# Optimization experiments

Measured on AMD Instinct MI355X. Metric: run time of the kernel, lower is better.

## Reference

```python
import jax, jax.numpy as jnp
import numpy as np

EMBED_DIM = 1024
NUM_HEADS = 16
HEAD_DIM = EMBED_DIM // NUM_HEADS
B, S = 4, 2048
LN_EPS = 1e-6


def setup_inputs() -> dict:
    key = jax.random.key(0)
    ks = jax.random.split(key, 11)
    sc = 1.0 / np.sqrt(EMBED_DIM)
    inputs = jax.random.normal(ks[0], (B, S, EMBED_DIM), dtype=jnp.float32)
    Wq = jax.random.normal(ks[1], (EMBED_DIM, EMBED_DIM), dtype=jnp.float32) * sc
    bq = jnp.zeros((EMBED_DIM,), jnp.float32)
    Wk = jax.random.normal(ks[2], (EMBED_DIM, EMBED_DIM), dtype=jnp.float32) * sc
    bk = jnp.zeros((EMBED_DIM,), jnp.float32)
    Wv = jax.random.normal(ks[3], (EMBED_DIM, EMBED_DIM), dtype=jnp.float32) * sc
    bv = jnp.zeros((EMBED_DIM,), jnp.float32)
    Wo = jax.random.normal(ks[4], (EMBED_DIM, EMBED_DIM), dtype=jnp.float32) * sc
    bo = jnp.zeros((EMBED_DIM,), jnp.float32)
    gamma = jnp.ones((EMBED_DIM,), jnp.float32)
    beta = jnp.zeros((EMBED_DIM,), jnp.float32)
    return {"inputs": inputs, "Wq": Wq, "bq": bq, "Wk": Wk, "bk": bk,
            "Wv": Wv, "bv": bv, "Wo": Wo, "bo": bo, "gamma": gamma, "beta": beta}


def _attention(inputs, Wq, bq, Wk, bk, Wv, bv, Wo, bo, gamma, beta):
    b, s, d = inputs.shape
    q = (inputs @ Wq + bq).reshape(b, s, NUM_HEADS, HEAD_DIM)
    k = (inputs @ Wk + bk).reshape(b, s, NUM_HEADS, HEAD_DIM)
    v = (inputs @ Wv + bv).reshape(b, s, NUM_HEADS, HEAD_DIM)
    scale = jnp.float32(np.sqrt(HEAD_DIM))
    # [b, h, s, s]
    scores = jnp.einsum('bqhd,bkhd->bhqk', q, k) / scale
    causal = jnp.tril(jnp.ones((s, s), dtype=bool))  # [s, s]
    scores = jnp.where(causal, scores, jnp.float32(-1e9))
    weights = jax.nn.softmax(scores, axis=-1)
    # dropout is identity at inference (training=False)
    attn = jnp.einsum('bhqk,bkhd->bqhd', weights, v).reshape(b, s, d)
    out = attn @ Wo + bo
    resid = inputs + out
    mu = jnp.mean(resid, axis=-1, keepdims=True)
    var = jnp.mean(jnp.square(resid - mu), axis=-1, keepdims=True)
    normed = (resid - mu) / jnp.sqrt(var + LN_EPS) * gamma + beta
    return normed, weights


def reference(inputs, Wq, bq, Wk, bk, Wv, bv, Wo, bo, gamma, beta):
    return _attention(inputs, Wq, bq, Wk, bk, Wv, bv, Wo, bo, gamma, beta)
```

## Files before the change

kernel.cpp:

```cpp
#include <hip/hip_runtime.h>
#include <math.h>

#define B_  4
#define S_  2048
#define D_  1024
#define H_  16
#define DH_ 64
#define M_  (B_*S_)
#define LN_EPS 1e-6f

typedef __attribute__((ext_vector_type(4))) float f32x4;
typedef __attribute__((ext_vector_type(8))) short s16x8;

__device__ __forceinline__ void split2(float x, ushort& h, ushort& l) {
  unsigned u = __float_as_uint(x);
  h = (ushort)(u >> 16);
  float r = x - __uint_as_float(u & 0xFFFF0000u);
  l = (ushort)(__float_as_uint(r) >> 16);
}

__global__ __launch_bounds__(256) void split_kernel(
    const float* __restrict__ in, ushort* __restrict__ hi, ushort* __restrict__ lo)
{
  const size_t t = (size_t)blockIdx.x * 256 + threadIdx.x;
  const float4 a = *(const float4*)(in + t * 8);
  const float4 b = *(const float4*)(in + t * 8 + 4);
  s16x8 hv, lv;
  ushort h, l;
  split2(a.x, h, l); hv[0] = (short)h; lv[0] = (short)l;
  split2(a.y, h, l); hv[1] = (short)h; lv[1] = (short)l;
  split2(a.z, h, l); hv[2] = (short)h; lv[2] = (short)l;
  split2(a.w, h, l); hv[3] = (short)h; lv[3] = (short)l;
  split2(b.x, h, l); hv[4] = (short)h; lv[4] = (short)l;
  split2(b.y, h, l); hv[5] = (short)h; lv[5] = (short)l;
  split2(b.z, h, l); hv[6] = (short)h; lv[6] = (short)l;
  split2(b.w, h, l); hv[7] = (short)h; lv[7] = (short)l;
  *(s16x8*)(hi + t * 8) = hv;
  *(s16x8*)(lo + t * 8) = lv;
}

__global__ __launch_bounds__(256) void splitT_kernel(
    const float* __restrict__ W, ushort* __restrict__ hiT, ushort* __restrict__ loT)
{
  __shared__ float tile[64][65];
  const int n0 = blockIdx.x * 64, k0 = blockIdx.y * 64;
  const int tid = threadIdx.x;
  #pragma unroll
  for (int i = 0; i < 4; ++i) {
    int c = tid + (i << 8);
    int r = c >> 4;
    int c4 = (c & 15) << 2;
    float4 v = *(const float4*)(W + (size_t)(k0 + r) * D_ + n0 + c4);
    tile[r][c4+0] = v.x; tile[r][c4+1] = v.y; tile[r][c4+2] = v.z; tile[r][c4+3] = v.w;
  }
  __syncthreads();
  #pragma unroll
  for (int i = 0; i < 4; ++i) {
    int c = tid + (i << 8);
    int n = c >> 4;
    int k4 = (c & 15) << 2;
    ushort h0,h1,h2,h3, l0,l1,l2,l3;
    split2(tile[k4+0][n], h0, l0);
    split2(tile[k4+1][n], h1, l1);
    split2(tile[k4+2][n], h2, l2);
    split2(tile[k4+3][n], h3, l3);
    size_t o = (size_t)(n0 + n) * D_ + k0 + k4;
    *(ushort4*)(hiT + o) = make_ushort4(h0, h1, h2, h3);
    *(ushort4*)(loT + o) = make_ushort4(l0, l1, l2, l3);
  }
}

#define LDK 40

__global__ __launch_bounds__(256) void gemm_mfma_kernel(
    const ushort* __restrict__ Ahi, const ushort* __restrict__ Alo,
    const ushort* __restrict__ BThi, const ushort* __restrict__ BTlo,
    const float* __restrict__ bias, const float* __restrict__ resid,
    float* __restrict__ C, int M, int N, int K)
{
  __shared__ ushort Ah[128][LDK];
  __shared__ ushort Al[128][LDK];
  __shared__ ushort Bh[128][LDK];
  __shared__ ushort Bl[128][LDK];
  const int tid  = threadIdx.x;
  const int lane = tid & 63;
  const int wid  = tid >> 6;
  const int wm   = wid >> 1, wn = wid & 1;
  const int bm = blockIdx.y * 128, bn = blockIdx.x * 128;

  const int c0 = tid,       r0 = c0 >> 2, k80 = (c0 & 3) << 3;
  const int c1 = tid + 256, r1 = c1 >> 2, k81 = (c1 & 3) << 3;

  f32x4 acc[4][4] = {};

  const int kf = (lane >> 4) << 3;
  const int fm = wm * 64 + (lane & 15);
  const int fn = wn * 64 + (lane & 15);

  for (int k0 = 0; k0 < K; k0 += 32) {
    const size_t ga0 = (size_t)(bm + r0) * K + k0 + k80;
    const size_t ga1 = (size_t)(bm + r1) * K + k0 + k81;
    const size_t gb0 = (size_t)(bn + r0) * K + k0 + k80;
    const size_t gb1 = (size_t)(bn + r1) * K + k0 + k81;
    s16x8 va0 = *(const s16x8*)(Ahi  + ga0);
    s16x8 va1 = *(const s16x8*)(Ahi  + ga1);
    s16x8 ua0 = *(const s16x8*)(Alo  + ga0);
    s16x8 ua1 = *(const s16x8*)(Alo  + ga1);
    s16x8 vb0 = *(const s16x8*)(BThi + gb0);
    s16x8 vb1 = *(const s16x8*)(BThi + gb1);
    s16x8 ub0 = *(const s16x8*)(BTlo + gb0);
    s16x8 ub1 = *(const s16x8*)(BTlo + gb1);
    *(s16x8*)&Ah[r0][k80] = va0;  *(s16x8*)&Ah[r1][k81] = va1;
    *(s16x8*)&Al[r0][k80] = ua0;  *(s16x8*)&Al[r1][k81] = ua1;
    *(s16x8*)&Bh[r0][k80] = vb0;  *(s16x8*)&Bh[r1][k81] = vb1;
    *(s16x8*)&Bl[r0][k80] = ub0;  *(s16x8*)&Bl[r1][k81] = ub1;
    __syncthreads();
    s16x8 ah[4], al[4], bh[4], bl[4];
    #pragma unroll
    for (int i = 0; i < 4; ++i) {
      ah[i] = *(const s16x8*)&Ah[fm + i*16][kf];
      al[i] = *(const s16x8*)&Al[fm + i*16][kf];
      bh[i] = *(const s16x8*)&Bh[fn + i*16][kf];
      bl[i] = *(const s16x8*)&Bl[fn + i*16][kf];
    }
    #pragma unroll
    for (int mi = 0; mi < 4; ++mi) {
      #pragma unroll
      for (int ni = 0; ni < 4; ++ni) {
        acc[mi][ni] = __builtin_amdgcn_mfma_f32_16x16x32_bf16(ah[mi], bh[ni], acc[mi][ni], 0, 0, 0);
        acc[mi][ni] = __builtin_amdgcn_mfma_f32_16x16x32_bf16(al[mi], bh[ni], acc[mi][ni], 0, 0, 0);
        acc[mi][ni] = __builtin_amdgcn_mfma_f32_16x16x32_bf16(ah[mi], bl[ni], acc[mi][ni], 0, 0, 0);
      }
    }
    __syncthreads();
  }
  const int rbase = bm + wm*64 + ((lane >> 4) << 2);
  #pragma unroll
  for (int ni = 0; ni < 4; ++ni) {
    const int col = bn + wn*64 + ni*16 + (lane & 15);
    const float bb = bias[col];
    #pragma unroll
    for (int mi = 0; mi < 4; ++mi) {
      #pragma unroll
      for (int j = 0; j < 4; ++j) {
        const int row = rbase + mi*16 + j;
        float v = acc[mi][ni][j] + bb;
        if (resid) v += resid[(size_t)row * N + col];
        C[(size_t)row * N + col] = v;
      }
    }
  }
}

__device__ __forceinline__ float block_allreduce(float v, bool is_max, float* sbuf) {
  #pragma unroll
  for (int o = 32; o > 0; o >>= 1) {
    float other = __shfl_down(v, o, 64);
    v = is_max ? fmaxf(v, other) : (v + other);
  }
  __syncthreads();
  if ((threadIdx.x & 63) == 0) sbuf[threadIdx.x >> 6] = v;
  __syncthreads();
  float r = sbuf[0];
  #pragma unroll
  for (int w = 1; w < 4; ++w) r = is_max ? fmaxf(r, sbuf[w]) : (r + sbuf[w]);
  return r;
}

__global__ __launch_bounds__(256) void scores_kernel(
    const float* __restrict__ Q, const float* __restrict__ Km,
    float* __restrict__ Wout)
{
  const int kt = blockIdx.x, qt = blockIdx.y;
  if (kt > qt) return;
  const int bh = blockIdx.z;
  const int b = bh >> 4, h = bh & 15;
  const int q0 = qt * 64, k0 = kt * 64;
  __shared__ float Qs[64][68];
  __shared__ float Ks[64][68];
  const int tid = threadIdx.x;
  const int tx = tid & 15, ty = tid >> 4;
  const float* Qbase = Q  + ((size_t)b * S_ + q0) * D_ + h * DH_;
  const float* Kbase = Km + ((size_t)b * S_ + k0) * D_ + h * DH_;
  #pragma unroll
  for (int i = 0; i < 4; ++i) {
    int idx = tid + i * 256;
    int r = idx >> 4;
    int c4 = (idx & 15) << 2;
    float4 qv = *(const float4*)(Qbase + (size_t)r * D_ + c4);
    *(float4*)(&Qs[r][c4]) = qv;
    float4 kv = *(const float4*)(Kbase + (size_t)r * D_ + c4);
    Ks[c4+0][r] = kv.x; Ks[c4+1][r] = kv.y; Ks[c4+2][r] = kv.z; Ks[c4+3][r] = kv.w;
  }
  __syncthreads();
  float acc[4][4] = {};
  #pragma unroll 8
  for (int d = 0; d < 64; ++d) {
    float4 kv = *(float4*)(&Ks[d][tx*4]);
    float a0 = Qs[ty*4+0][d], a1 = Qs[ty*4+1][d];
    float a2 = Qs[ty*4+2][d], a3 = Qs[ty*4+3][d];
    acc[0][0] += a0*kv.x; acc[0][1] += a0*kv.y; acc[0][2] += a0*kv.z; acc[0][3] += a0*kv.w;
    acc[1][0] += a1*kv.x; acc[1][1] += a1*kv.y; acc[1][2] += a1*kv.z; acc[1][3] += a1*kv.w;
    acc[2][0] += a2*kv.x; acc[2][1] += a2*kv.y; acc[2][2] += a2*kv.z; acc[2][3] += a2*kv.w;
    acc[3][0] += a3*kv.x; acc[3][1] += a3*kv.y; acc[3][2] += a3*kv.z; acc[3][3] += a3*kv.w;
  }
  const float scale = 0.125f;
  float* Wrow = Wout + ((size_t)bh * S_ + q0) * S_ + k0;
  if (kt < qt) {
    #pragma unroll
    for (int i = 0; i < 4; ++i) {
      float4 o;
      o.x = acc[i][0]*scale; o.y = acc[i][1]*scale;
      o.z = acc[i][2]*scale; o.w = acc[i][3]*scale;
      *(float4*)(Wrow + (size_t)(ty*4+i) * S_ + tx*4) = o;
    }
  } else {
    #pragma unroll
    for (int i = 0; i < 4; ++i) {
      int qg = q0 + ty*4 + i;
      #pragma unroll
      for (int j = 0; j < 4; ++j) {
        int kg = k0 + tx*4 + j;
        if (kg <= qg) Wrow[(size_t)(ty*4+i) * S_ + tx*4 + j] = acc[i][j] * scale;
      }
    }
  }
}

__global__ __launch_bounds__(256) void softmax_kernel(float* __restrict__ Wbuf) {
  const int q = blockIdx.x;
  float* row = Wbuf + ((size_t)blockIdx.y * S_ + q) * S_;
  const int valid = q + 1;
  __shared__ float sbuf[4];
  float v[8];
  float lmax = -INFINITY;
  #pragma unroll
  for (int i = 0; i < 8; ++i) {
    int k = threadIdx.x + (i << 8);
    v[i] = (k < valid) ? row[k] : -INFINITY;
    lmax = fmaxf(lmax, v[i]);
  }
  float m = block_allreduce(lmax, true, sbuf);
  float lsum = 0.f;
  #pragma unroll
  for (int i = 0; i < 8; ++i) {
    int k = threadIdx.x + (i << 8);
    v[i] = (k < valid) ? __expf(v[i] - m) : 0.f;
    lsum += v[i];
  }
  float s = block_allreduce(lsum, false, sbuf);
  float inv = 1.f / s;
  #pragma unroll
  for (int i = 0; i < 8; ++i) {
    int k = threadIdx.x + (i << 8);
    row[k] = v[i] * inv;
  }
}

__global__ __launch_bounds__(256) void pv_kernel(
    const float* __restrict__ Wbuf, const float* __restrict__ V,
    float* __restrict__ Attn)
{
  const int qt = blockIdx.x, h = blockIdx.y, b = blockIdx.z;
  const int q0 = qt * 64;
  __shared__ float Ws[64][68];
  __shared__ float Vs[64][68];
  const int tid = threadIdx.x;
  const int tx = tid & 15, ty = tid >> 4;
  float acc[4][4] = {};
  const size_t wbase = (((size_t)b * H_ + h) * S_ + q0) * S_;
  const float* Vbase = V + (size_t)b * S_ * D_ + h * DH_;
  for (int kt = 0; kt <= qt; ++kt) {
    int k0 = kt * 64;
    #pragma unroll
    for (int i = 0; i < 4; ++i) {
      int idx = tid + i * 256;
      int r = idx >> 4, c4 = (idx & 15) << 2;
      *(float4*)(&Ws[r][c4]) = *(const float4*)(Wbuf + wbase + (size_t)r * S_ + k0 + c4);
      *(float4*)(&Vs[r][c4]) = *(const float4*)(Vbase + (size_t)(k0 + r) * D_ + c4);
    }
    __syncthreads();
    #pragma unroll 8
    for (int kk = 0; kk < 64; ++kk) {
      float4 vv = *(float4*)(&Vs[kk][tx*4]);
      float w0 = Ws[ty*4+0][kk], w1 = Ws[ty*4+1][kk];
      float w2 = Ws[ty*4+2][kk], w3 = Ws[ty*4+3][kk];
      acc[0][0] += w0*vv.x; acc[0][1] += w0*vv.y; acc[0][2] += w0*vv.z; acc[0][3] += w0*vv.w;
      acc[1][0] += w1*vv.x; acc[1][1] += w1*vv.y; acc[1][2] += w1*vv.z; acc[1][3] += w1*vv.w;
      acc[2][0] += w2*vv.x; acc[2][1] += w2*vv.y; acc[2][2] += w2*vv.z; acc[2][3] += w2*vv.w;
      acc[3][0] += w3*vv.x; acc[3][1] += w3*vv.y; acc[3][2] += w3*vv.z; acc[3][3] += w3*vv.w;
    }
    __syncthreads();
  }
  #pragma unroll
  for (int i = 0; i < 4; ++i) {
    float4 o = { acc[i][0], acc[i][1], acc[i][2], acc[i][3] };
    *(float4*)(Attn + ((size_t)b * S_ + q0 + ty*4 + i) * D_ + h * DH_ + tx*4) = o;
  }
}

__global__ __launch_bounds__(256) void ln_kernel(
    const float* __restrict__ R, const float* __restrict__ gamma,
    const float* __restrict__ beta, float* __restrict__ Out)
{
  const int row = blockIdx.x;
  const float* x = R + (size_t)row * D_;
  __shared__ float sbuf[4];
  float4 xv = *(const float4*)(x + threadIdx.x * 4);
  float s  = xv.x + xv.y + xv.z + xv.w;
  float ss = xv.x*xv.x + xv.y*xv.y + xv.z*xv.z + xv.w*xv.w;
  float tot  = block_allreduce(s,  false, sbuf);
  float tot2 = block_allreduce(ss, false, sbuf);
  float mu  = tot  * (1.f / D_);
  float var = tot2 * (1.f / D_) - mu * mu;
  float inv = rsqrtf(var + LN_EPS);
  float4 g  = *(const float4*)(gamma + threadIdx.x * 4);
  float4 be = *(const float4*)(beta  + threadIdx.x * 4);
  float4 o;
  o.x = (xv.x - mu) * inv * g.x + be.x;
  o.y = (xv.y - mu) * inv * g.y + be.y;
  o.z = (xv.z - mu) * inv * g.z + be.z;
  o.w = (xv.w - mu) * inv * g.w + be.w;
  *(float4*)(Out + (size_t)row * D_ + threadIdx.x * 4) = o;
}

extern "C" void kernel_launch(void* const* d_in, const int* in_sizes, int n_in,
                              void* d_out, int out_size, void* d_ws, size_t ws_size,
                              hipStream_t stream) {
  const float* X     = (const float*)d_in[0];
  const float* Wq    = (const float*)d_in[1];
  const float* bq    = (const float*)d_in[2];
  const float* Wk    = (const float*)d_in[3];
  const float* bk    = (const float*)d_in[4];
  const float* Wv    = (const float*)d_in[5];
  const float* bv    = (const float*)d_in[6];
  const float* Wo    = (const float*)d_in[7];
  const float* bo    = (const float*)d_in[8];
  const float* gamma = (const float*)d_in[9];
  const float* beta  = (const float*)d_in[10];

  float* out     = (float*)d_out;
  float* normed  = out;
  float* weights = out + (size_t)B_ * S_ * D_;

  const size_t sz = (size_t)B_ * S_ * D_;
  const size_t wsz = (size_t)D_ * D_;
  float* ws   = (float*)d_ws;
  float* Qb   = ws;
  float* Kb   = ws + sz;
  float* Vb   = ws + 2 * sz;
  float* Attn  = Qb;
  float* Resid = Kb;

  ushort* Xhi  = (ushort*)weights;
  ushort* Xlo  = Xhi + sz;
  ushort* WqHi = Xlo + sz;      ushort* WqLo = WqHi + wsz;
  ushort* WkHi = WqLo + wsz;    ushort* WkLo = WkHi + wsz;
  ushort* WvHi = WkLo + wsz;    ushort* WvLo = WvHi + wsz;
  ushort* AtHi = (ushort*)Vb;   ushort* AtLo = AtHi + sz;
  ushort* WoHi = (ushort*)Qb;   ushort* WoLo = WoHi + wsz;

  dim3 blk(256);
  dim3 gg(D_ / 128, M_ / 128);
  dim3 sg(sz / 2048);

  split_kernel <<<sg, blk, 0, stream>>>(X, Xhi, Xlo);
  splitT_kernel<<<dim3(16,16), blk, 0, stream>>>(Wq, WqHi, WqLo);
  splitT_kernel<<<dim3(16,16), blk, 0, stream>>>(Wk, WkHi, WkLo);
  splitT_kernel<<<dim3(16,16), blk, 0, stream>>>(Wv, WvHi, WvLo);

  gemm_mfma_kernel<<<gg, blk, 0, stream>>>(Xhi, Xlo, WqHi, WqLo, bq, nullptr, Qb, M_, D_, D_);
  gemm_mfma_kernel<<<gg, blk, 0, stream>>>(Xhi, Xlo, WkHi, WkLo, bk, nullptr, Kb, M_, D_, D_);
  gemm_mfma_kernel<<<gg, blk, 0, stream>>>(Xhi, Xlo, WvHi, WvLo, bv, nullptr, Vb, M_, D_, D_);

  scores_kernel<<<dim3(S_/64, S_/64, B_*H_), blk, 0, stream>>>(Qb, Kb, weights);
  softmax_kernel<<<dim3(S_, B_*H_), blk, 0, stream>>>(weights);
  pv_kernel<<<dim3(S_/64, H_, B_), blk, 0, stream>>>(weights, Vb, Attn);

  split_kernel <<<sg, blk, 0, stream>>>(Attn, AtHi, AtLo);
  splitT_kernel<<<dim3(16,16), blk, 0, stream>>>(Wo, WoHi, WoLo);
  gemm_mfma_kernel<<<gg, blk, 0, stream>>>(AtHi, AtLo, WoHi, WoLo, bo, X, Resid, M_, D_, D_);

  ln_kernel<<<dim3(M_), blk, 0, stream>>>(Resid, gamma, beta, normed);
}
```

Measured before the change: 2.339 ms.

## Move attention scores and PV products to split-bf16 MFMA kernels

Replaces the scalar FP32 scores and PV kernels with MFMA versions. Each fp32 operand is split into bf16 hi and lo parts in shared memory and combined with three MFMAs to keep near-fp32 accuracy. Query tiles grow to 128 rows, with the causal mask handled per 64-wide key tile. This trades FMA-bound compute for matrix-core throughput, at the cost of extra split arithmetic, more LDS traffic and scattered scalar stores for the output.

```diff
diff --git a/kernel.cpp b/kernel.cpp
--- a/kernel.cpp
+++ b/kernel.cpp
@@ -167,61 +167,100 @@
   return r;
 }
 
-__global__ __launch_bounds__(256) void scores_kernel(
+#define SQP 72
+
+__global__ __launch_bounds__(256) void scores_mfma_kernel(
     const float* __restrict__ Q, const float* __restrict__ Km,
     float* __restrict__ Wout)
 {
-  const int kt = blockIdx.x, qt = blockIdx.y;
-  if (kt > qt) return;
+  const int kt = blockIdx.x;
+  const int qt = blockIdx.y;
+  if (kt > 2*qt + 1) return;
   const int bh = blockIdx.z;
   const int b = bh >> 4, h = bh & 15;
-  const int q0 = qt * 64, k0 = kt * 64;
-  __shared__ float Qs[64][68];
-  __shared__ float Ks[64][68];
+  const int q0 = qt * 128, k0 = kt * 64;
+  __shared__ ushort Qh[128][SQP], Ql[128][SQP];
+  __shared__ ushort Kh[64][SQP],  Kl[64][SQP];
   const int tid = threadIdx.x;
-  const int tx = tid & 15, ty = tid >> 4;
+  const int lane = tid & 63, wid = tid >> 6;
+  const int wm = wid >> 1, wn = wid & 1;
   const float* Qbase = Q  + ((size_t)b * S_ + q0) * D_ + h * DH_;
   const float* Kbase = Km + ((size_t)b * S_ + k0) * D_ + h * DH_;
   #pragma unroll
+  for (int i = 0; i < 8; ++i) {
+    int idx = tid + (i << 8);
+    int r = idx >> 4, c4 = (idx & 15) << 2;
+    float4 v = *(const float4*)(Qbase + (size_t)r * D_ + c4);
+    ushort h0,h1,h2,h3,l0,l1,l2,l3;
+    split2(v.x,h0,l0); split2(v.y,h1,l1); split2(v.z,h2,l2); split2(v.w,h3,l3);
+    *(ushort4*)&Qh[r][c4] = make_ushort4(h0,h1,h2,h3);
+    *(ushort4*)&Ql[r][c4] = make_ushort4(l0,l1,l2,l3);
+  }
+  #pragma unroll
   for (int i = 0; i < 4; ++i) {
-    int idx = tid + i * 256;
-    int r = idx >> 4;
-    int c4 = (idx & 15) << 2;
-    float4 qv = *(const float4*)(Qbase + (size_t)r * D_ + c4);
-    *(float4*)(&Qs[r][c4]) = qv;
-    float4 kv = *(const float4*)(Kbase + (size_t)r * D_ + c4);
-    Ks[c4+0][r] = kv.x; Ks[c4+1][r] = kv.y; Ks[c4+2][r] = kv.z; Ks[c4+3][r] = kv.w;
+    int idx = tid + (i << 8);
+    int r = idx >> 4, c4 = (idx & 15) << 2;
+    float4 v = *(const float4*)(Kbase + (size_t)r * D_ + c4);
+    ushort h0,h1,h2,h3,l0,l1,l2,l3;
+    split2(v.x,h0,l0); split2(v.y,h1,l1); split2(v.z,h2,l2); split2(v.w,h3,l3);
+    *(ushort4*)&Kh[r][c4] = make_ushort4(h0,h1,h2,h3);
+    *(ushort4*)&Kl[r][c4] = make_ushort4(l0,l1,l2,l3);
   }
   __syncthreads();
-  float acc[4][4] = {};
-  #pragma unroll 8
-  for (int d = 0; d < 64; ++d) {
-    float4 kv = *(float4*)(&Ks[d][tx*4]);
-    float a0 = Qs[ty*4+0][d], a1 = Qs[ty*4+1][d];
-    float a2 = Qs[ty*4+2][d], a3 = Qs[ty*4+3][d];
-    acc[0][0] += a0*kv.x; acc[0][1] += a0*kv.y; acc[0][2] += a0*kv.z; acc[0][3] += a0*kv.w;
-    acc[1][0] += a1*kv.x; acc[1][1] += a1*kv.y; acc[1][2] += a1*kv.z; acc[1][3] += a1*kv.w;
-    acc[2][0] += a2*kv.x; acc[2][1] += a2*kv.y; acc[2][2] += a2*kv.z; acc[2][3] += a2*kv.w;
-    acc[3][0] += a3*kv.x; acc[3][1] += a3*kv.y; acc[3][2] += a3*kv.z; acc[3][3] += a3*kv.w;
+  const int kf = (lane >> 4) << 3;
+  const int fm = wm * 64 + (lane & 15);
+  const int fn = wn * 32 + (lane & 15);
+  f32x4 acc[4][2] = {};
+  #pragma unroll
+  for (int d0 = 0; d0 < 64; d0 += 32) {
+    s16x8 qa[4], qb[4], ka[2], kb[2];
+    #pragma unroll
+    for (int mi = 0; mi < 4; ++mi) {
+      qa[mi] = *(const s16x8*)&Qh[fm + mi*16][d0 + kf];
+      qb[mi] = *(const s16x8*)&Ql[fm + mi*16][d0 + kf];
+    }
+    #pragma unroll
+    for (int ni = 0; ni < 2; ++ni) {
+      ka[ni] = *(const s16x8*)&Kh[fn + ni*16][d0 + kf];
+      kb[ni] = *(const s16x8*)&Kl[fn + ni*16][d0 + kf];
+    }
+    #pragma unroll
+    for (int mi = 0; mi < 4; ++mi) {
+      #pragma unroll
+      for (int ni = 0; ni < 2; ++ni) {
+        acc[mi][ni] = __builtin_amdgcn_mfma_f32_16x16x32_bf16(qa[mi], ka[ni], acc[mi][ni], 0, 0, 0);
+        acc[mi][ni] = __builtin_amdgcn_mfma_f32_16x16x32_bf16(qb[mi], ka[ni], acc[mi][ni], 0, 0, 0);
+        acc[mi][ni] = __builtin_amdgcn_mfma_f32_16x16x32_bf16(qa[mi], kb[ni], acc[mi][ni], 0, 0, 0);
+      }
+    }
   }
   const float scale = 0.125f;
   float* Wrow = Wout + ((size_t)bh * S_ + q0) * S_ + k0;
-  if (kt < qt) {
-    #pragma unroll
-    for (int i = 0; i < 4; ++i) {
-      float4 o;
-      o.x = acc[i][0]*scale; o.y = acc[i][1]*scale;
-      o.z = acc[i][2]*scale; o.w = acc[i][3]*scale;
-      *(float4*)(Wrow + (size_t)(ty*4+i) * S_ + tx*4) = o;
+  const int rb = wm*64 + ((lane >> 4) << 2);
+  if ((kt >> 1) < qt) {
+    #pragma unroll
+    for (int ni = 0; ni < 2; ++ni) {
+      const int col = wn*32 + ni*16 + (lane & 15);
+      #pragma unroll
+      for (int mi = 0; mi < 4; ++mi) {
+        #pragma unroll
+        for (int j = 0; j < 4; ++j)
+          Wrow[(size_t)(rb + mi*16 + j) * S_ + col] = acc[mi][ni][j] * scale;
+      }
     }
   } else {
     #pragma unroll
-    for (int i = 0; i < 4; ++i) {
-      int qg = q0 + ty*4 + i;
-      #pragma unroll
-      for (int j = 0; j < 4; ++j) {
-        int kg = k0 + tx*4 + j;
-        if (kg <= qg) Wrow[(size_t)(ty*4+i) * S_ + tx*4 + j] = acc[i][j] * scale;
+    for (int ni = 0; ni < 2; ++ni) {
+      const int col = wn*32 + ni*16 + (lane & 15);
+      const int kg = k0 + col;
+      #pragma unroll
+      for (int mi = 0; mi < 4; ++mi) {
+        #pragma unroll
+        for (int j = 0; j < 4; ++j) {
+          const int row = rb + mi*16 + j;
+          if (kg <= q0 + row)
+            Wrow[(size_t)row * S_ + col] = acc[mi][ni][j] * scale;
+        }
       }
     }
   }
@@ -257,45 +296,85 @@
   }
 }
 
-__global__ __launch_bounds__(256) void pv_kernel(
+#define PVW 72
+#define PVV 74
+
+__global__ __launch_bounds__(256) void pv_mfma_kernel(
     const float* __restrict__ Wbuf, const float* __restrict__ V,
     float* __restrict__ Attn)
 {
   const int qt = blockIdx.x, h = blockIdx.y, b = blockIdx.z;
-  const int q0 = qt * 64;
-  __shared__ float Ws[64][68];
-  __shared__ float Vs[64][68];
+  const int q0 = qt * 128;
+  __shared__ ushort Wh[128][PVW], Wl[128][PVW];
+  __shared__ ushort Vh[64][PVV],  Vl[64][PVV];
   const int tid = threadIdx.x;
-  const int tx = tid & 15, ty = tid >> 4;
-  float acc[4][4] = {};
+  const int lane = tid & 63, wid = tid >> 6;
+  const int wm = wid >> 1, wn = wid & 1;
+  f32x4 acc[4][2] = {};
   const size_t wbase = (((size_t)b * H_ + h) * S_ + q0) * S_;
   const float* Vbase = V + (size_t)b * S_ * D_ + h * DH_;
-  for (int kt = 0; kt <= qt; ++kt) {
-    int k0 = kt * 64;
+  const int kf = (lane >> 4) << 3;
+  const int fm = wm * 64 + (lane & 15);
+  const int fn = wn * 32 + (lane & 15);
+  const int nkt = 2*qt + 2;
+  for (int kt = 0; kt < nkt; ++kt) {
+    const int k0 = kt * 64;
+    #pragma unroll
+    for (int i = 0; i < 8; ++i) {
+      int idx = tid + (i << 8);
+      int r = idx >> 4, c4 = (idx & 15) << 2;
+      float4 v = *(const float4*)(Wbuf + wbase + (size_t)r * S_ + k0 + c4);
+      ushort h0,h1,h2,h3,l0,l1,l2,l3;
+      split2(v.x,h0,l0); split2(v.y,h1,l1); split2(v.z,h2,l2); split2(v.w,h3,l3);
+      *(ushort4*)&Wh[r][c4] = make_ushort4(h0,h1,h2,h3);
+      *(ushort4*)&Wl[r][c4] = make_ushort4(l0,l1,l2,l3);
+    }
     #pragma unroll
     for (int i = 0; i < 4; ++i) {
-      int idx = tid + i * 256;
+      int idx = tid + (i << 8);
       int r = idx >> 4, c4 = (idx & 15) << 2;
-      *(float4*)(&Ws[r][c4]) = *(const float4*)(Wbuf + wbase + (size_t)r * S_ + k0 + c4);
-      *(float4*)(&Vs[r][c4]) = *(const float4*)(Vbase + (size_t)(k0 + r) * D_ + c4);
+      float4 v = *(const float4*)(Vbase + (size_t)(k0 + r) * D_ + c4);
+      ushort h0,h1,h2,h3,l0,l1,l2,l3;
+      split2(v.x,h0,l0); split2(v.y,h1,l1); split2(v.z,h2,l2); split2(v.w,h3,l3);
+      Vh[c4+0][r] = h0; Vh[c4+1][r] = h1; Vh[c4+2][r] = h2; Vh[c4+3][r] = h3;
+      Vl[c4+0][r] = l0; Vl[c4+1][r] = l1; Vl[c4+2][r] = l2; Vl[c4+3][r] = l3;
     }
     __syncthreads();
-    #pragma unroll 8
-    for (int kk = 0; kk < 64; ++kk) {
-      float4 vv = *(float4*)(&Vs[kk][tx*4]);
-      float w0 = Ws[ty*4+0][kk], w1 = Ws[ty*4+1][kk];
-      float w2 = Ws[ty*4+2][kk], w3 = Ws[ty*4+3][kk];
-      acc[0][0] += w0*vv.x; acc[0][1] += w0*vv.y; acc[0][2] += w0*vv.z; acc[0][3] += w0*vv.w;
-      acc[1][0] += w1*vv.x; acc[1][1] += w1*vv.y; acc[1][2] += w1*vv.z; acc[1][3] += w1*vv.w;
-      acc[2][0] += w2*vv.x; acc[2][1] += w2*vv.y; acc[2][2] += w2*vv.z; acc[2][3] += w2*vv.w;
-      acc[3][0] += w3*vv.x; acc[3][1] += w3*vv.y; acc[3][2] += w3*vv.z; acc[3][3] += w3*vv.w;
+    #pragma unroll
+    for (int kk = 0; kk < 64; kk += 32) {
+      s16x8 wa[4], wb[4], va[2], vb[2];
+      #pragma unroll
+      for (int mi = 0; mi < 4; ++mi) {
+        wa[mi] = *(const s16x8*)&Wh[fm + mi*16][kk + kf];
+        wb[mi] = *(const s16x8*)&Wl[fm + mi*16][kk + kf];
+      }
+      #pragma unroll
+      for (int ni = 0; ni < 2; ++ni) {
+        va[ni] = *(const s16x8*)&Vh[fn + ni*16][kk + kf];
+        vb[ni] = *(const s16x8*)&Vl[fn + ni*16][kk + kf];
+      }
+      #pragma unroll
+      for (int mi = 0; mi < 4; ++mi) {
+        #pragma unroll
+        for (int ni = 0; ni < 2; ++ni) {
+          acc[mi][ni] = __builtin_amdgcn_mfma_f32_16x16x32_bf16(wa[mi], va[ni], acc[mi][ni], 0, 0, 0);
+          acc[mi][ni] = __builtin_amdgcn_mfma_f32_16x16x32_bf16(wb[mi], va[ni], acc[mi][ni], 0, 0, 0);
+          acc[mi][ni] = __builtin_amdgcn_mfma_f32_16x16x32_bf16(wa[mi], vb[ni], acc[mi][ni], 0, 0, 0);
+        }
+      }
     }
     __syncthreads();
   }
-  #pragma unroll
-  for (int i = 0; i < 4; ++i) {
-    float4 o = { acc[i][0], acc[i][1], acc[i][2], acc[i][3] };
-    *(float4*)(Attn + ((size_t)b * S_ + q0 + ty*4 + i) * D_ + h * DH_ + tx*4) = o;
+  const int rb = q0 + wm*64 + ((lane >> 4) << 2);
+  #pragma unroll
+  for (int ni = 0; ni < 2; ++ni) {
+    const int col = h * DH_ + wn*32 + ni*16 + (lane & 15);
+    #pragma unroll
+    for (int mi = 0; mi < 4; ++mi) {
+      #pragma unroll
+      for (int j = 0; j < 4; ++j)
+        Attn[((size_t)b * S_ + rb + mi*16 + j) * D_ + col] = acc[mi][ni][j];
+    }
   }
 }
 
@@ -373,9 +452,9 @@
   gemm_mfma_kernel<<<gg, blk, 0, stream>>>(Xhi, Xlo, WkHi, WkLo, bk, nullptr, Kb, M_, D_, D_);
   gemm_mfma_kernel<<<gg, blk, 0, stream>>>(Xhi, Xlo, WvHi, WvLo, bv, nullptr, Vb, M_, D_, D_);
 
-  scores_kernel<<<dim3(S_/64, S_/64, B_*H_), blk, 0, stream>>>(Qb, Kb, weights);
+  scores_mfma_kernel<<<dim3(S_/64, S_/128, B_*H_), blk, 0, stream>>>(Qb, Kb, weights);
   softmax_kernel<<<dim3(S_, B_*H_), blk, 0, stream>>>(weights);
-  pv_kernel<<<dim3(S_/64, H_, B_), blk, 0, stream>>>(weights, Vb, Attn);
+  pv_mfma_kernel<<<dim3(S_/128, H_, B_), blk, 0, stream>>>(weights, Vb, Attn);
 
   split_kernel <<<sg, blk, 0, stream>>>(Attn, AtHi, AtLo);
   splitT_kernel<<<dim3(16,16), blk, 0, stream>>>(Wo, WoHi, WoLo);
```

Measured after the change: 2.122 ms. 1.1x faster.

## Fuse scores, softmax and PV into flash-style MFMA attention kernel; async LDS loads in GEMM

Applied to the files above, without the earlier changes.

Replaces the separate scores, softmax and PV kernels with one flash-attention style kernel. It uses split-bf16 MFMA for QK^T and PV with an online softmax, then recomputes the scores in a second pass to write the normalized weights and zero the masked region. This avoids writing, rereading and rewriting the full score matrix across three kernels, at the cost of computing QK^T twice. The GEMM also switches to global_load_lds direct-to-LDS loads without padding, which may add LDS bank conflicts. Note that Attn aliases Qb, but each block reads only its own Q rows into registers before writing Attn.

```diff
diff --git a/kernel.cpp b/kernel.cpp
--- a/kernel.cpp
+++ b/kernel.cpp
@@ -11,6 +11,12 @@
 
 typedef __attribute__((ext_vector_type(4))) float f32x4;
 typedef __attribute__((ext_vector_type(8))) short s16x8;
+
+__device__ __forceinline__ void gl16(const void* g, void* l) {
+  __builtin_amdgcn_global_load_lds(
+      (const __attribute__((address_space(1))) unsigned int*)g,
+      (__attribute__((address_space(3))) unsigned int*)l, 16, 0, 0);
+}
 
 __device__ __forceinline__ void split2(float x, ushort& h, ushort& l) {
   unsigned u = __float_as_uint(x);
@@ -70,50 +76,48 @@
   }
 }
 
-#define LDK 40
-
 __global__ __launch_bounds__(256) void gemm_mfma_kernel(
     const ushort* __restrict__ Ahi, const ushort* __restrict__ Alo,
     const ushort* __restrict__ BThi, const ushort* __restrict__ BTlo,
     const float* __restrict__ bias, const float* __restrict__ resid,
     float* __restrict__ C, int M, int N, int K)
 {
-  __shared__ ushort Ah[128][LDK];
-  __shared__ ushort Al[128][LDK];
-  __shared__ ushort Bh[128][LDK];
-  __shared__ ushort Bl[128][LDK];
+  __shared__ ushort Ah[128][32], Al[128][32], Bh[128][32], Bl[128][32];
   const int tid  = threadIdx.x;
   const int lane = tid & 63;
   const int wid  = tid >> 6;
   const int wm   = wid >> 1, wn = wid & 1;
   const int bm = blockIdx.y * 128, bn = blockIdx.x * 128;
 
-  const int c0 = tid,       r0 = c0 >> 2, k80 = (c0 & 3) << 3;
-  const int c1 = tid + 256, r1 = c1 >> 2, k81 = (c1 & 3) << 3;
+  const int j0 = wid * 128 + lane, j1 = j0 + 64;
+  const int r0 = j0 >> 2, kc0 = (j0 & 3) << 3;
+  const int r1 = j1 >> 2, kc1 = (j1 & 3) << 3;
+  const unsigned off0 = (unsigned)(wid * 128) * 16;
+  const unsigned off1 = off0 + 1024;
+
+  const ushort* a0  = Ahi  + (size_t)(bm + r0) * K + kc0;
+  const ushort* a1  = Ahi  + (size_t)(bm + r1) * K + kc1;
+  const ushort* c0  = Alo  + (size_t)(bm + r0) * K + kc0;
+  const ushort* c1  = Alo  + (size_t)(bm + r1) * K + kc1;
+  const ushort* b0  = BThi + (size_t)(bn + r0) * K + kc0;
+  const ushort* b1  = BThi + (size_t)(bn + r1) * K + kc1;
+  const ushort* d0p = BTlo + (size_t)(bn + r0) * K + kc0;
+  const ushort* d1p = BTlo + (size_t)(bn + r1) * K + kc1;
 
   f32x4 acc[4][4] = {};
-
   const int kf = (lane >> 4) << 3;
   const int fm = wm * 64 + (lane & 15);
   const int fn = wn * 64 + (lane & 15);
 
   for (int k0 = 0; k0 < K; k0 += 32) {
-    const size_t ga0 = (size_t)(bm + r0) * K + k0 + k80;
-    const size_t ga1 = (size_t)(bm + r1) * K + k0 + k81;
-    const size_t gb0 = (size_t)(bn + r0) * K + k0 + k80;
-    const size_t gb1 = (size_t)(bn + r1) * K + k0 + k81;
-    s16x8 va0 = *(const s16x8*)(Ahi  + ga0);
-    s16x8 va1 = *(const s16x8*)(Ahi  + ga1);
-    s16x8 ua0 = *(const s16x8*)(Alo  + ga0);
-    s16x8 ua1 = *(const s16x8*)(Alo  + ga1);
-    s16x8 vb0 = *(const s16x8*)(BThi + gb0);
-    s16x8 vb1 = *(const s16x8*)(BThi + gb1);
-    s16x8 ub0 = *(const s16x8*)(BTlo + gb0);
-    s16x8 ub1 = *(const s16x8*)(BTlo + gb1);
-    *(s16x8*)&Ah[r0][k80] = va0;  *(s16x8*)&Ah[r1][k81] = va1;
-    *(s16x8*)&Al[r0][k80] = ua0;  *(s16x8*)&Al[r1][k81] = ua1;
-    *(s16x8*)&Bh[r0][k80] = vb0;  *(s16x8*)&Bh[r1][k81] = vb1;
-    *(s16x8*)&Bl[r0][k80] = ub0;  *(s16x8*)&Bl[r1][k81] = ub1;
+    gl16(a0 + k0,  (char*)&Ah[0][0] + off0);
+    gl16(a1 + k0,  (char*)&Ah[0][0] + off1);
+    gl16(c0 + k0,  (char*)&Al[0][0] + off0);
+    gl16(c1 + k0,  (char*)&Al[0][0] + off1);
+    gl16(b0 + k0,  (char*)&Bh[0][0] + off0);
+    gl16(b1 + k0,  (char*)&Bh[0][0] + off1);
+    gl16(d0p + k0, (char*)&Bl[0][0] + off0);
+    gl16(d1p + k0, (char*)&Bl[0][0] + off1);
     __syncthreads();
     s16x8 ah[4], al[4], bh[4], bl[4];
     #pragma unroll
@@ -152,6 +156,197 @@
   }
 }
 
+__global__ __launch_bounds__(256) void attn_fused_kernel(
+    const float* Q, const float* __restrict__ Kg, const float* __restrict__ Vg,
+    float* __restrict__ Wout, float* Attn)
+{
+  const int qt = blockIdx.x, h = blockIdx.y, b = blockIdx.z;
+  const int q0 = qt * 64;
+  __shared__ ushort Kh[64][72], Kl[64][72];
+  __shared__ ushort Vh[64][72], Vl[64][72];
+  const int tid = threadIdx.x;
+  const int lane = tid & 63, w = tid >> 6;
+  const int l15 = lane & 15, lg = lane >> 4;
+  const int kf = lg << 3;
+
+  const float* Qrow = Q + ((size_t)(b * S_ + q0 + w*16 + l15)) * D_ + h * DH_;
+  s16x8 qh[2], ql[2];
+  #pragma unroll
+  for (int hd = 0; hd < 2; ++hd) {
+    float x[8];
+    *(float4*)&x[0] = *(const float4*)(Qrow + hd*32 + kf);
+    *(float4*)&x[4] = *(const float4*)(Qrow + hd*32 + kf + 4);
+    #pragma unroll
+    for (int e = 0; e < 8; ++e) {
+      ushort hh, ll; split2(x[e], hh, ll);
+      qh[hd][e] = (short)hh; ql[hd][e] = (short)ll;
+    }
+  }
+
+  float mrow[4], lrow[4];
+  #pragma unroll
+  for (int j = 0; j < 4; ++j) { mrow[j] = -INFINITY; lrow[j] = 0.f; }
+  f32x4 acc[4] = {};
+
+  const float* Kbase = Kg + (size_t)b * S_ * D_ + h * DH_;
+  const float* Vbase = Vg + (size_t)b * S_ * D_ + h * DH_;
+  const int nkt = qt + 1;
+
+  for (int kt = 0; kt < nkt; ++kt) {
+    const int k0 = kt * 64;
+    __syncthreads();
+    #pragma unroll
+    for (int i = 0; i < 4; ++i) {
+      int idx = tid + (i << 8);
+      int r = idx >> 4, c4 = (idx & 15) << 2;
+      float4 kv = *(const float4*)(Kbase + (size_t)(k0 + r) * D_ + c4);
+      ushort h0,h1,h2,h3,l0,l1,l2,l3;
+      split2(kv.x,h0,l0); split2(kv.y,h1,l1); split2(kv.z,h2,l2); split2(kv.w,h3,l3);
+      *(ushort4*)&Kh[r][c4] = make_ushort4(h0,h1,h2,h3);
+      *(ushort4*)&Kl[r][c4] = make_ushort4(l0,l1,l2,l3);
+      float4 vv = *(const float4*)(Vbase + (size_t)(k0 + r) * D_ + c4);
+      split2(vv.x,h0,l0); split2(vv.y,h1,l1); split2(vv.z,h2,l2); split2(vv.w,h3,l3);
+      Vh[c4+0][r]=h0; Vh[c4+1][r]=h1; Vh[c4+2][r]=h2; Vh[c4+3][r]=h3;
+      Vl[c4+0][r]=l0; Vl[c4+1][r]=l1; Vl[c4+2][r]=l2; Vl[c4+3][r]=l3;
+    }
+    __syncthreads();
+    f32x4 s[4] = {};
+    #pragma unroll
+    for (int hd = 0; hd < 2; ++hd) {
+      #pragma unroll
+      for (int ni = 0; ni < 4; ++ni) {
+        s16x8 ka = *(const s16x8*)&Kh[ni*16 + l15][hd*32 + kf];
+        s16x8 kb = *(const s16x8*)&Kl[ni*16 + l15][hd*32 + kf];
+        s[ni] = __builtin_amdgcn_mfma_f32_16x16x32_bf16(qh[hd], ka, s[ni], 0, 0, 0);
+        s[ni] = __builtin_amdgcn_mfma_f32_16x16x32_bf16(ql[hd], ka, s[ni], 0, 0, 0);
+        s[ni] = __builtin_amdgcn_mfma_f32_16x16x32_bf16(qh[hd], kb, s[ni], 0, 0, 0);
+      }
+    }
+    __syncthreads();
+    const bool diag = (kt == qt);
+    float sv[4][4];
+    #pragma unroll
+    for (int ni = 0; ni < 4; ++ni) {
+      #pragma unroll
+      for (int j = 0; j < 4; ++j) {
+        float x = s[ni][j] * 0.125f;
+        if (diag && (ni*16 + l15 > w*16 + lg*4 + j)) x = -INFINITY;
+        sv[ni][j] = x;
+      }
+    }
+    float fac[4];
+    #pragma unroll
+    for (int j = 0; j < 4; ++j) {
+      float t = fmaxf(fmaxf(sv[0][j], sv[1][j]), fmaxf(sv[2][j], sv[3][j]));
+      #pragma unroll
+      for (int o = 1; o < 16; o <<= 1) t = fmaxf(t, __shfl_xor(t, o, 64));
+      float mn = fmaxf(mrow[j], t);
+      fac[j] = __expf(mrow[j] - mn);
+      mrow[j] = mn;
+    }
+    float p[4][4];
+    #pragma unroll
+    for (int ni = 0; ni < 4; ++ni)
+      #pragma unroll
+      for (int j = 0; j < 4; ++j)
+        p[ni][j] = __expf(sv[ni][j] - mrow[j]);
+    #pragma unroll
+    for (int j = 0; j < 4; ++j) {
+      float su = p[0][j] + p[1][j] + p[2][j] + p[3][j];
+      #pragma unroll
+      for (int o = 1; o < 16; o <<= 1) su += __shfl_xor(su, o, 64);
+      lrow[j] = lrow[j] * fac[j] + su;
+    }
+    #pragma unroll
+    for (int nd = 0; nd < 4; ++nd)
+      #pragma unroll
+      for (int j = 0; j < 4; ++j)
+        acc[nd][j] *= fac[j];
+    #pragma unroll
+    for (int ni = 0; ni < 4; ++ni)
+      #pragma unroll
+      for (int j = 0; j < 4; ++j) {
+        ushort hh, ll; split2(p[ni][j], hh, ll);
+        Kh[w*16 + lg*4 + j][ni*16 + l15] = hh;
+        Kl[w*16 + lg*4 + j][ni*16 + l15] = ll;
+      }
+    #pragma unroll
+    for (int hd = 0; hd < 2; ++hd) {
+      s16x8 pa = *(const s16x8*)&Kh[w*16 + l15][hd*32 + kf];
+      s16x8 pb = *(const s16x8*)&Kl[w*16 + l15][hd*32 + kf];
+      #pragma unroll
+      for (int nd = 0; nd < 4; ++nd) {
+        s16x8 va = *(const s16x8*)&Vh[nd*16 + l15][hd*32 + kf];
+        s16x8 vb = *(const s16x8*)&Vl[nd*16 + l15][hd*32 + kf];
+        acc[nd] = __builtin_amdgcn_mfma_f32_16x16x32_bf16(pa, va, acc[nd], 0, 0, 0);
+        acc[nd] = __builtin_amdgcn_mfma_f32_16x16x32_bf16(pb, va, acc[nd], 0, 0, 0);
+        acc[nd] = __builtin_amdgcn_mfma_f32_16x16x32_bf16(pa, vb, acc[nd], 0, 0, 0);
+      }
+    }
+  }
+
+  float invl[4];
+  #pragma unroll
+  for (int j = 0; j < 4; ++j) invl[j] = 1.f / lrow[j];
+  #pragma unroll
+  for (int nd = 0; nd < 4; ++nd)
+    #pragma unroll
+    for (int j = 0; j < 4; ++j)
+      Attn[((size_t)(b * S_ + q0 + w*16 + lg*4 + j)) * D_ + h * DH_ + nd*16 + l15]
+          = acc[nd][j] * invl[j];
+
+  float* Wrow = Wout + (((size_t)(b * H_ + h)) * S_ + q0) * S_;
+  for (int kt = 0; kt < nkt; ++kt) {
+    const int k0 = kt * 64;
+    __syncthreads();
+    #pragma unroll
+    for (int i = 0; i < 4; ++i) {
+      int idx = tid + (i << 8);
+      int r = idx >> 4, c4 = (idx & 15) << 2;
+      float4 kv = *(const float4*)(Kbase + (size_t)(k0 + r) * D_ + c4);
+      ushort h0,h1,h2,h3,l0,l1,l2,l3;
+      split2(kv.x,h0,l0); split2(kv.y,h1,l1); split2(kv.z,h2,l2); split2(kv.w,h3,l3);
+      *(ushort4*)&Kh[r][c4] = make_ushort4(h0,h1,h2,h3);
+      *(ushort4*)&Kl[r][c4] = make_ushort4(l0,l1,l2,l3);
+    }
+    __syncthreads();
+    f32x4 s[4] = {};
+    #pragma unroll
+    for (int hd = 0; hd < 2; ++hd) {
+      #pragma unroll
+      for (int ni = 0; ni < 4; ++ni) {
+        s16x8 ka = *(const s16x8*)&Kh[ni*16 + l15][hd*32 + kf];
+        s16x8 kb = *(const s16x8*)&Kl[ni*16 + l15][hd*32 + kf];
+        s[ni] = __builtin_amdgcn_mfma_f32_16x16x32_bf16(qh[hd], ka, s[ni], 0, 0, 0);
+        s[ni] = __builtin_amdgcn_mfma_f32_16x16x32_bf16(ql[hd], ka, s[ni], 0, 0, 0);
+        s[ni] = __builtin_amdgcn_mfma_f32_16x16x32_bf16(qh[hd], kb, s[ni], 0, 0, 0);
+      }
+    }
+    const bool diag = (kt == qt);
+    #pragma unroll
+    for (int ni = 0; ni < 4; ++ni) {
+      #pragma unroll
+      for (int j = 0; j < 4; ++j) {
+        float x = s[ni][j] * 0.125f;
+        float wv;
+        if (diag && (ni*16 + l15 > w*16 + lg*4 + j)) wv = 0.f;
+        else wv = __expf(x - mrow[j]) * invl[j];
+        Wrow[(size_t)(w*16 + lg*4 + j) * S_ + k0 + ni*16 + l15] = wv;
+      }
+    }
+  }
+  for (int kt = nkt; kt < S_/64; ++kt) {
+    const int k0 = kt * 64;
+    #pragma unroll
+    for (int i = 0; i < 4; ++i) {
+      int idx = tid + (i << 8);
+      int r = idx >> 4, c4 = (idx & 15) << 2;
+      float4 z = {0.f, 0.f, 0.f, 0.f};
+      *(float4*)(Wrow + (size_t)r * S_ + k0 + c4) = z;
+    }
+  }
+}
+
 __device__ __forceinline__ float block_allreduce(float v, bool is_max, float* sbuf) {
   #pragma unroll
   for (int o = 32; o > 0; o >>= 1) {
@@ -165,138 +360,6 @@
   #pragma unroll
   for (int w = 1; w < 4; ++w) r = is_max ? fmaxf(r, sbuf[w]) : (r + sbuf[w]);
   return r;
-}
-
-__global__ __launch_bounds__(256) void scores_kernel(
-    const float* __restrict__ Q, const float* __restrict__ Km,
-    float* __restrict__ Wout)
-{
-  const int kt = blockIdx.x, qt = blockIdx.y;
-  if (kt > qt) return;
-  const int bh = blockIdx.z;
-  const int b = bh >> 4, h = bh & 15;
-  const int q0 = qt * 64, k0 = kt * 64;
-  __shared__ float Qs[64][68];
-  __shared__ float Ks[64][68];
-  const int tid = threadIdx.x;
-  const int tx = tid & 15, ty = tid >> 4;
-  const float* Qbase = Q  + ((size_t)b * S_ + q0) * D_ + h * DH_;
-  const float* Kbase = Km + ((size_t)b * S_ + k0) * D_ + h * DH_;
-  #pragma unroll
-  for (int i = 0; i < 4; ++i) {
-    int idx = tid + i * 256;
-    int r = idx >> 4;
-    int c4 = (idx & 15) << 2;
-    float4 qv = *(const float4*)(Qbase + (size_t)r * D_ + c4);
-    *(float4*)(&Qs[r][c4]) = qv;
-    float4 kv = *(const float4*)(Kbase + (size_t)r * D_ + c4);
-    Ks[c4+0][r] = kv.x; Ks[c4+1][r] = kv.y; Ks[c4+2][r] = kv.z; Ks[c4+3][r] = kv.w;
-  }
-  __syncthreads();
-  float acc[4][4] = {};
-  #pragma unroll 8
-  for (int d = 0; d < 64; ++d) {
-    float4 kv = *(float4*)(&Ks[d][tx*4]);
-    float a0 = Qs[ty*4+0][d], a1 = Qs[ty*4+1][d];
-    float a2 = Qs[ty*4+2][d], a3 = Qs[ty*4+3][d];
-    acc[0][0] += a0*kv.x; acc[0][1] += a0*kv.y; acc[0][2] += a0*kv.z; acc[0][3] += a0*kv.w;
-    acc[1][0] += a1*kv.x; acc[1][1] += a1*kv.y; acc[1][2] += a1*kv.z; acc[1][3] += a1*kv.w;
-    acc[2][0] += a2*kv.x; acc[2][1] += a2*kv.y; acc[2][2] += a2*kv.z; acc[2][3] += a2*kv.w;
-    acc[3][0] += a3*kv.x; acc[3][1] += a3*kv.y; acc[3][2] += a3*kv.z; acc[3][3] += a3*kv.w;
-  }
-  const float scale = 0.125f;
-  float* Wrow = Wout + ((size_t)bh * S_ + q0) * S_ + k0;
-  if (kt < qt) {
-    #pragma unroll
-    for (int i = 0; i < 4; ++i) {
-      float4 o;
-      o.x = acc[i][0]*scale; o.y = acc[i][1]*scale;
-      o.z = acc[i][2]*scale; o.w = acc[i][3]*scale;
-      *(float4*)(Wrow + (size_t)(ty*4+i) * S_ + tx*4) = o;
-    }
-  } else {
-    #pragma unroll
-    for (int i = 0; i < 4; ++i) {
-      int qg = q0 + ty*4 + i;
-      #pragma unroll
-      for (int j = 0; j < 4; ++j) {
-        int kg = k0 + tx*4 + j;
-        if (kg <= qg) Wrow[(size_t)(ty*4+i) * S_ + tx*4 + j] = acc[i][j] * scale;
-      }
-    }
-  }
-}
-
-__global__ __launch_bounds__(256) void softmax_kernel(float* __restrict__ Wbuf) {
-  const int q = blockIdx.x;
-  float* row = Wbuf + ((size_t)blockIdx.y * S_ + q) * S_;
-  const int valid = q + 1;
-  __shared__ float sbuf[4];
-  float v[8];
-  float lmax = -INFINITY;
-  #pragma unroll
-  for (int i = 0; i < 8; ++i) {
-    int k = threadIdx.x + (i << 8);
-    v[i] = (k < valid) ? row[k] : -INFINITY;
-    lmax = fmaxf(lmax, v[i]);
-  }
-  float m = block_allreduce(lmax, true, sbuf);
-  float lsum = 0.f;
-  #pragma unroll
-  for (int i = 0; i < 8; ++i) {
-    int k = threadIdx.x + (i << 8);
-    v[i] = (k < valid) ? __expf(v[i] - m) : 0.f;
-    lsum += v[i];
-  }
-  float s = block_allreduce(lsum, false, sbuf);
-  float inv = 1.f / s;
-  #pragma unroll
-  for (int i = 0; i < 8; ++i) {
-    int k = threadIdx.x + (i << 8);
-    row[k] = v[i] * inv;
-  }
-}
-
-__global__ __launch_bounds__(256) void pv_kernel(
-    const float* __restrict__ Wbuf, const float* __restrict__ V,
-    float* __restrict__ Attn)
-{
-  const int qt = blockIdx.x, h = blockIdx.y, b = blockIdx.z;
-  const int q0 = qt * 64;
-  __shared__ float Ws[64][68];
-  __shared__ float Vs[64][68];
-  const int tid = threadIdx.x;
-  const int tx = tid & 15, ty = tid >> 4;
-  float acc[4][4] = {};
-  const size_t wbase = (((size_t)b * H_ + h) * S_ + q0) * S_;
-  const float* Vbase = V + (size_t)b * S_ * D_ + h * DH_;
-  for (int kt = 0; kt <= qt; ++kt) {
-    int k0 = kt * 64;
-    #pragma unroll
-    for (int i = 0; i < 4; ++i) {
-      int idx = tid + i * 256;
-      int r = idx >> 4, c4 = (idx & 15) << 2;
-      *(float4*)(&Ws[r][c4]) = *(const float4*)(Wbuf + wbase + (size_t)r * S_ + k0 + c4);
-      *(float4*)(&Vs[r][c4]) = *(const float4*)(Vbase + (size_t)(k0 + r) * D_ + c4);
-    }
-    __syncthreads();
-    #pragma unroll 8
-    for (int kk = 0; kk < 64; ++kk) {
-      float4 vv = *(float4*)(&Vs[kk][tx*4]);
-      float w0 = Ws[ty*4+0][kk], w1 = Ws[ty*4+1][kk];
-      float w2 = Ws[ty*4+2][kk], w3 = Ws[ty*4+3][kk];
-      acc[0][0] += w0*vv.x; acc[0][1] += w0*vv.y; acc[0][2] += w0*vv.z; acc[0][3] += w0*vv.w;
-      acc[1][0] += w1*vv.x; acc[1][1] += w1*vv.y; acc[1][2] += w1*vv.z; acc[1][3] += w1*vv.w;
-      acc[2][0] += w2*vv.x; acc[2][1] += w2*vv.y; acc[2][2] += w2*vv.z; acc[2][3] += w2*vv.w;
-      acc[3][0] += w3*vv.x; acc[3][1] += w3*vv.y; acc[3][2] += w3*vv.z; acc[3][3] += w3*vv.w;
-    }
-    __syncthreads();
-  }
-  #pragma unroll
-  for (int i = 0; i < 4; ++i) {
-    float4 o = { acc[i][0], acc[i][1], acc[i][2], acc[i][3] };
-    *(float4*)(Attn + ((size_t)b * S_ + q0 + ty*4 + i) * D_ + h * DH_ + tx*4) = o;
-  }
 }
 
 __global__ __launch_bounds__(256) void ln_kernel(
@@ -345,6 +408,7 @@
 
   const size_t sz = (size_t)B_ * S_ * D_;
   const size_t wsz = (size_t)D_ * D_;
+
   float* ws   = (float*)d_ws;
   float* Qb   = ws;
   float* Kb   = ws + sz;
@@ -352,13 +416,13 @@
   float* Attn  = Qb;
   float* Resid = Kb;
 
-  ushort* Xhi  = (ushort*)weights;
-  ushort* Xlo  = Xhi + sz;
-  ushort* WqHi = Xlo + sz;      ushort* WqLo = WqHi + wsz;
-  ushort* WkHi = WqLo + wsz;    ushort* WkLo = WkHi + wsz;
-  ushort* WvHi = WkLo + wsz;    ushort* WvLo = WvHi + wsz;
-  ushort* AtHi = (ushort*)Vb;   ushort* AtLo = AtHi + sz;
-  ushort* WoHi = (ushort*)Qb;   ushort* WoLo = WoHi + wsz;
+  ushort* w0   = (ushort*)weights;
+  ushort* Xhi  = w0;           ushort* Xlo  = w0 + sz;
+  ushort* WqHi = w0 + 2*sz;    ushort* WqLo = WqHi + wsz;
+  ushort* WkHi = WqLo + wsz;   ushort* WkLo = WkHi + wsz;
+  ushort* WvHi = WkLo + wsz;   ushort* WvLo = WvHi + wsz;
+  ushort* AtHi = (ushort*)Vb;  ushort* AtLo = AtHi + sz;
+  ushort* WoHi = (ushort*)Qb;  ushort* WoLo = WoHi + wsz;
 
   dim3 blk(256);
   dim3 gg(D_ / 128, M_ / 128);
@@ -373,9 +437,7 @@
   gemm_mfma_kernel<<<gg, blk, 0, stream>>>(Xhi, Xlo, WkHi, WkLo, bk, nullptr, Kb, M_, D_, D_);
   gemm_mfma_kernel<<<gg, blk, 0, stream>>>(Xhi, Xlo, WvHi, WvLo, bv, nullptr, Vb, M_, D_, D_);
 
-  scores_kernel<<<dim3(S_/64, S_/64, B_*H_), blk, 0, stream>>>(Qb, Kb, weights);
-  softmax_kernel<<<dim3(S_, B_*H_), blk, 0, stream>>>(weights);
-  pv_kernel<<<dim3(S_/64, H_, B_), blk, 0, stream>>>(weights, Vb, Attn);
+  attn_fused_kernel<<<dim3(S_/64, H_, B_), blk, 0, stream>>>(Qb, Kb, Vb, weights, Attn);
 
   split_kernel <<<sg, blk, 0, stream>>>(Attn, AtHi, AtLo);
   splitT_kernel<<<dim3(16,16), blk, 0, stream>>>(Wo, WoHi, WoLo);
```

Measured after the change: 2.024 ms. -13.5%, faster.
